# Optimization experiments

Hardware: AMD Instinct MI355X
Metric: run time of the kernel (lower is better)

## Reference

```python
import jax, jax.numpy as jnp
import numpy as np

C_IN, C_OUT, K, STRIDE, PAD = 64, 64, 3, 1, 1


def setup_inputs() -> dict:
    key = jax.random.key(0)
    k0, k1, k2, k3, k4 = jax.random.split(key, 5)
    x = jax.random.normal(k0, (8, C_IN, 128, 128), jnp.float32)
    # offset conv: out_channels = 2*K*K (torch inits to 0; use small random for non-trivial offsets)
    w_off = jax.random.normal(k1, (2 * K * K, C_IN, K, K), jnp.float32) * 0.01
    b_off = jax.random.normal(k2, (2 * K * K,), jnp.float32) * 0.01
    w_conv = jax.random.normal(k3, (C_OUT, C_IN, K, K), jnp.float32) * float(1.0 / np.sqrt(C_IN * K * K))
    b_conv = jax.random.normal(k4, (C_OUT,), jnp.float32) * 0.01
    return {"x": x, "w_off": w_off, "b_off": b_off, "w_conv": w_conv, "b_conv": b_conv}


def _conv(x, w, b, stride):
    y = jax.lax.conv_general_dilated(
        x, w, (stride, stride), 'VALID', dimension_numbers=('NCHW', 'OIHW', 'NCHW'))
    return y + b[None, :, None, None]


def _deform_forward(x, w_off, b_off, w_conv, b_conv):
    n, c, H, W = x.shape
    ph = H + 2 * PAD  # padded (square) spatial size
    xp = jnp.pad(x, ((0, 0), (0, 0), (PAD, PAD), (PAD, PAD)))
    offset = _conv(xp, w_off, b_off, STRIDE)           # [n, 2*K*K, h, w]
    h, w = offset.shape[2], offset.shape[3]
    # channel layout in the torch code: first K*K channels = x (col) deltas, next K*K = y (row)
    off = offset.reshape(n, 2, K, K, h, w)             # [n, {x,y}, ki, kj, h, w]
    base = (PAD + STRIDE * jnp.arange(h)).astype(x.dtype)          # p_0 centers in padded coords
    rng = (jnp.arange(K) - (K - 1) // 2).astype(x.dtype)           # p_n kernel offsets
    cx = off[:, 0] + base[None, None, None, None, :] + rng[None, None, :, None, None]
    cy = off[:, 1] + base[None, None, None, :, None] + rng[None, :, None, None, None]
    # equivalent to grid*2/(ph-1)-1 clamped to [-1,1] with align_corners=True
    cx = jnp.clip(cx, 0.0, ph - 1)
    cy = jnp.clip(cy, 0.0, ph - 1)
    # reorder [n, ki, kj, h, w] -> [n, h, ki, w, kj] -> [n, h*K, w*K] (matches torch permutes)
    cx = cx.transpose(0, 3, 1, 4, 2).reshape(n, h * K, w * K)
    cy = cy.transpose(0, 3, 1, 4, 2).reshape(n, h * K, w * K)
    # bilinear sampling (grid_sample, align_corners=True)
    x0 = jnp.floor(cx); y0 = jnp.floor(cy)
    wx = cx - x0; wy = cy - y0
    x0i = x0.astype(jnp.int32); y0i = y0.astype(jnp.int32)
    x1i = jnp.minimum(x0i + 1, ph - 1); y1i = jnp.minimum(y0i + 1, ph - 1)
    xf = xp.reshape(n, c, ph * ph)
    gather = jax.vmap(lambda xb, ib: xb[:, ib])        # ([c, P], [Hk, Wk]) -> [c, Hk, Wk]
    g00 = gather(xf, y0i * ph + x0i)
    g01 = gather(xf, y0i * ph + x1i)
    g10 = gather(xf, y1i * ph + x0i)
    g11 = gather(xf, y1i * ph + x1i)
    wxb = wx[:, None]; wyb = wy[:, None]               # broadcast over channels
    samp = (g00 * (1 - wxb) * (1 - wyb) + g01 * wxb * (1 - wyb)
            + g10 * (1 - wxb) * wyb + g11 * wxb * wyb)  # [n, c, h*K, w*K]
    return _conv(samp, w_conv, b_conv, K)               # stride-K conv -> [n, C_OUT, h, w]


def reference(x, w_off, b_off, w_conv, b_conv):
    return _deform_forward(x, w_off, b_off, w_conv, b_conv)
```

## Files before the change

### kernel.cpp

```cpp
#include <hip/hip_runtime.h>
#include <hip/hip_bf16.h>


#define PH   130
#define CIN  64
#define COUT 64
#define WROWS 7
#define WCOLS 72
#define ROWB  (WCOLS * 128)
#define WINB  (WROWS * ROWB)

typedef __attribute__((ext_vector_type(8))) __bf16 bf16x8;
typedef __attribute__((ext_vector_type(4))) float  f32x4;

__device__ __forceinline__ short f2bf(float f) {
  return __builtin_bit_cast(short, __float2bfloat16(f));
}
__device__ __forceinline__ float blo(unsigned u) {
  return __builtin_bit_cast(float, u << 16);
}
__device__ __forceinline__ float bhi(unsigned u) {
  return __builtin_bit_cast(float, u & 0xffff0000u);
}
__device__ __forceinline__ unsigned packbf(float a, float b) {
  unsigned lo16 = (unsigned short)__builtin_bit_cast(unsigned short, __float2bfloat16(a));
  unsigned hi16 = (unsigned short)__builtin_bit_cast(unsigned short, __float2bfloat16(b));
  return lo16 | (hi16 << 16);
}

__global__ __launch_bounds__(256) void k_pad_prep(
    const float* __restrict__ x, const float* __restrict__ w_off,
    const float* __restrict__ w_conv, __hip_bfloat16* __restrict__ xpT,
    short* __restrict__ Bpack, short* __restrict__ wOffPack) {
  __shared__ __hip_bfloat16 tile[128 * 64];
  int bid = blockIdx.x;
  int tid = threadIdx.x;
  if (bid < 8 * PH) {
    int n = bid / PH;
    int y = bid % PH;
    bool interior = (y >= 1 && y <= 128);
    if (interior) {
      for (int i = tid; i < 2048; i += 256) {
        int c  = i >> 5;
        int w4 = (i & 31) << 2;
        float4 v = *(const float4*)(x + (((size_t)(n * 64 + c) * 128) + (y - 1)) * 128 + w4);
        int sw = (i & 7) << 3;
        tile[(w4 + 0) * 64 + (c ^ sw)] = __float2bfloat16(v.x);
        tile[(w4 + 1) * 64 + (c ^ sw)] = __float2bfloat16(v.y);
        tile[(w4 + 2) * 64 + (c ^ sw)] = __float2bfloat16(v.z);
        tile[(w4 + 3) * 64 + (c ^ sw)] = __float2bfloat16(v.w);
      }
    }
    __syncthreads();
    __hip_bfloat16* dst = xpT + (size_t)(n * PH + y) * PH * CIN;
    bool zrow = (y == 0 || y == PH - 1);
    for (int i = tid; i < 1040; i += 256) {
      int px = i >> 3;
      int c0 = (i & 7) << 3;
      uint4 v;
      if (zrow || px == 0 || px == PH - 1) {
        v = make_uint4(0u, 0u, 0u, 0u);
      } else {
        int pxi = px - 1;
        int c0s = c0 ^ (((pxi >> 2) & 7) << 3);
        v = *(const uint4*)&tile[pxi * 64 + c0s];
      }
      *(uint4*)(dst + (size_t)i * 8) = v;
    }
  } else {
    int t = (bid - 8 * PH) * 256 + tid;
    if (t < 18 * 4 * 64) {
      int lane = t & 63;
      int nt   = (t >> 6) & 3;
      int kk   = t >> 8;
      int co   = nt * 16 + (lane & 15);
      int kbase = kk * 32 + ((lane >> 4) << 3);
      short v[8];
#pragma unroll
      for (int i = 0; i < 8; ++i) {
        int k = kbase + i;
        v[i] = f2bf(w_conv[(size_t)(co * 64 + (k & 63)) * 9 + (k >> 6)]);
      }
      *(uint4*)(Bpack + (size_t)t * 8) = *(const uint4*)v;
    }
    int u = t - 18 * 4 * 64;
    if (u >= 0 && u < 18 * 2 * 64) {
      int lane = u & 63;
      int nt   = (u >> 6) & 1;
      int kk   = u >> 7;
      int co   = nt * 16 + (lane & 15);
      int kbase = kk * 32 + ((lane >> 4) << 3);
      short v[8];
#pragma unroll
      for (int i = 0; i < 8; ++i) {
        int k = kbase + i;
        v[i] = (co < 18) ? f2bf(w_off[(size_t)(co * 64 + (k & 63)) * 9 + (k >> 6)]) : (short)0;
      }
      *(uint4*)(wOffPack + (size_t)u * 8) = *(const uint4*)v;
    }
  }
}

__global__ __launch_bounds__(256, 2) void k_fused(
    const __hip_bfloat16* __restrict__ xpT, const short* __restrict__ Bpack,
    const short* __restrict__ wOffPack, const float* __restrict__ b_off,
    const float* __restrict__ b_conv, float* __restrict__ out) {
  __shared__ __attribute__((aligned(16))) char shraw[78912];
  char*  win     = shraw;
  float* offsLds = (float*)(shraw + WINB);
  int4*  metaLds = (int4*)(shraw + WINB + 5120);
  int*   tf      = (int*)(shraw + WINB + 5120 + 9216);
  float* olds    = (float*)shraw;

  int bid = blockIdx.x;
  int wh  = bid & 1;
  int h   = (bid >> 1) & 127;
  int n   = bid >> 8;
  int w0  = wh << 6;
  int tid = threadIdx.x, wv = tid >> 6, lane = tid & 63;
  int p = lane & 15, oct = lane >> 4;
  const char* xbB = (const char*)(xpT + (size_t)n * PH * PH * CIN);

  if (tid < 9) tf[tid] = 0;
  for (int i = tid; i < 4032; i += 256) {
    int rec = i >> 3, chunk = i & 7;
    int r = rec / WCOLS, c = rec - r * WCOLS;
    int wrow = h - 2 + r, wcol = w0 - 2 + c;
    if ((unsigned)wrow <= 129u && (unsigned)wcol <= 129u) {
      uint4 v = *(const uint4*)(xbB + (size_t)(wrow * 130 + wcol) * 128 + chunk * 16);
      *(uint4*)(win + rec * 128 + ((chunk * 16) ^ ((c & 7) << 4))) = v;
    }
  }
  __syncthreads();

  {
    f32x4 ao0 = {0.f, 0.f, 0.f, 0.f}, ao1 = ao0;
    const bf16x8* Wo = (const bf16x8*)wOffPack;
    int colbase = 2 + wv * 16 + p;
#pragma unroll
    for (int kk = 0; kk < 18; ++kk) {
      int tap = kk >> 1;
      int ky = tap / 3, kx = tap - (tap / 3) * 3;
      int sub = kk & 1;
      int col = colbase + kx;
      int addr = (2 + ky) * ROWB + col * 128 + ((oct * 16 + sub * 64) ^ ((col & 7) << 4));
      bf16x8 a  = *(const bf16x8*)(win + addr);
      bf16x8 b0 = Wo[(kk * 2 + 0) * 64 + lane];
      bf16x8 b1 = Wo[(kk * 2 + 1) * 64 + lane];
      ao0 = __builtin_amdgcn_mfma_f32_16x16x32_bf16(a, b0, ao0, 0, 0, 0);
      ao1 = __builtin_amdgcn_mfma_f32_16x16x32_bf16(a, b1, ao1, 0, 0, 0);
    }
    int co = lane & 15;
    float bo0 = b_off[co];
#pragma unroll
    for (int r = 0; r < 4; ++r)
      offsLds[(wv * 16 + oct * 4 + r) * 20 + co] = ao0[r] + bo0;
    if (co < 2) {
      float bo1 = b_off[16 + co];
#pragma unroll
      for (int r = 0; r < 4; ++r)
        offsLds[(wv * 16 + oct * 4 + r) * 20 + 16 + co] = ao1[r] + bo1;
    }
  }
  __syncthreads();

  for (int t = tid; t < 576; t += 256) {
    int pix = t / 9, tap = t - pix * 9;
    int ky = tap / 3, kx = tap - (tap / 3) * 3;
    float cx = offsLds[pix * 20 + tap]     + (float)(w0 + pix + kx);
    float cy = offsLds[pix * 20 + 9 + tap] + (float)(h + ky);
    cx = fminf(fmaxf(cx, 0.f), 129.f);
    cy = fminf(fmaxf(cy, 0.f), 129.f);
    float x0f = floorf(cx), y0f = floorf(cy);
    int x0i = (int)x0f, y0i = (int)y0f;
    float wx = cx - x0f, wy = cy - y0f;
    int x1i = min(x0i + 1, 129), y1i = min(y0i + 1, 129);
    int x0r = x0i - w0 + 2, y0r = y0i - h + 2;
    int x1r = x1i - w0 + 2, y1r = y1i - h + 2;
    bool inw = (x0r >= 0) && (y0r >= 0) && (x1r <= WCOLS - 1) && (y1r <= WROWS - 1);
    if (!inw) atomicOr(&tf[tap], 1);
    int dxr = x1i - x0i, dyr = y1i - y0i;
    int rec00 = (y0r * WCOLS + x0r) & 511;
    metaLds[t] = make_int4((y0i * 130 + x0i) << 7, __builtin_bit_cast(int, wx),
                           __builtin_bit_cast(int, wy),
                           rec00 | (dxr << 9) | (dyr << 10));
  }
  __syncthreads();

  f32x4 acc0 = {0.f, 0.f, 0.f, 0.f}, acc1 = acc0, acc2 = acc0, acc3 = acc0;
  const bf16x8* Bp = (const bf16x8*)Bpack;
  int mbase = (wv * 16 + p) * 9;
  int innerQ = oct * 16;
  for (int tap = 0; tap < 9; ++tap) {
    int tfv = tf[tap];
    int4 mt = metaLds[mbase + tap];
    float wx = __builtin_bit_cast(float, mt.y);
    float wy = __builtin_bit_cast(float, mt.z);
    float w11 = wx * wy;
    float w01 = wx - w11;
    float w10 = wy - w11;
    float w00 = 1.f - wx - w10;
    int wrd = mt.w;
    int dxr = (wrd >> 9) & 1, dyr = (wrd >> 10) & 1;
    int a00 = 0, a01 = 0, a10 = 0, a11 = 0;
    const char* pb = nullptr;
    int dx = 0, dy = 0;
    if (tfv == 0) {
      int r00 = wrd & 511;
      int r01 = r00 + dxr, r10 = r00 + WCOLS * dyr, r11 = r10 + dxr;
      a00 = r00 * 128 + (innerQ ^ ((r00 & 7) << 4));
      a01 = r01 * 128 + (innerQ ^ ((r01 & 7) << 4));
      a10 = r10 * 128 + (innerQ ^ ((r10 & 7) << 4));
      a11 = r11 * 128 + (innerQ ^ ((r11 & 7) << 4));
    } else {
      pb = xbB + mt.x + (oct << 4);
      dx = dxr << 7;
      dy = dyr * 16640;
    }
#pragma unroll
    for (int half = 0; half < 2; ++half) {
      uint4 q00, q01, q10, q11;
      if (tfv == 0) {
        int hx = half << 6;
        q00 = *(const uint4*)(win + (a00 ^ hx));
        q01 = *(const uint4*)(win + (a01 ^ hx));
        q10 = *(const uint4*)(win + (a10 ^ hx));
        q11 = *(const uint4*)(win + (a11 ^ hx));
      } else {
        const char* pc = pb + (half << 6);
        q00 = *(const uint4*)(pc);
        q01 = *(const uint4*)(pc + dx);
        q10 = *(const uint4*)(pc + dy);
        q11 = *(const uint4*)(pc + dx + dy);
      }
      unsigned av[4];
#pragma unroll
      for (int j = 0; j < 4; ++j) {
        unsigned u00 = ((const unsigned*)&q00)[j];
        unsigned u01 = ((const unsigned*)&q01)[j];
        unsigned u10 = ((const unsigned*)&q10)[j];
        unsigned u11 = ((const unsigned*)&q11)[j];
        float sl = blo(u00) * w00 + blo(u01) * w01 + blo(u10) * w10 + blo(u11) * w11;
        float sh = bhi(u00) * w00 + bhi(u01) * w01 + bhi(u10) * w10 + bhi(u11) * w11;
        av[j] = packbf(sl, sh);
      }
      bf16x8 a = __builtin_bit_cast(bf16x8, *(uint4*)av);
      int kk = tap * 2 + half;
      bf16x8 b0 = Bp[(kk * 4 + 0) * 64 + lane];
      bf16x8 b1 = Bp[(kk * 4 + 1) * 64 + lane];
      bf16x8 b2 = Bp[(kk * 4 + 2) * 64 + lane];
      bf16x8 b3 = Bp[(kk * 4 + 3) * 64 + lane];
      acc0 = __builtin_amdgcn_mfma_f32_16x16x32_bf16(a, b0, acc0, 0, 0, 0);
      acc1 = __builtin_amdgcn_mfma_f32_16x16x32_bf16(a, b1, acc1, 0, 0, 0);
      acc2 = __builtin_amdgcn_mfma_f32_16x16x32_bf16(a, b2, acc2, 0, 0, 0);
      acc3 = __builtin_amdgcn_mfma_f32_16x16x32_bf16(a, b3, acc3, 0, 0, 0);
    }
  }
  __syncthreads();

  int prow0 = wv * 16 + (oct << 2);
#pragma unroll
  for (int r = 0; r < 4; ++r) {
    olds[(prow0 + r) * 68 + p     ] = acc0[r];
    olds[(prow0 + r) * 68 + p + 16] = acc1[r];
    olds[(prow0 + r) * 68 + p + 32] = acc2[r];
    olds[(prow0 + r) * 68 + p + 48] = acc3[r];
  }
  __syncthreads();
  float* ob = out + (size_t)n * COUT * 16384 + (size_t)h * 128 + w0;
  for (int i = tid; i < 4096; i += 256) {
    int co = i >> 6, px = i & 63;
    ob[(size_t)co * 16384 + px] = olds[px * 68 + co] + b_conv[co];
  }
}

extern "C" void kernel_launch(void* const* d_in, const int* in_sizes, int n_in,
                              void* d_out, int out_size, void* d_ws, size_t ws_size,
                              hipStream_t stream) {
  const float* x      = (const float*)d_in[0];
  const float* w_off  = (const float*)d_in[1];
  const float* b_off  = (const float*)d_in[2];
  const float* w_conv = (const float*)d_in[3];
  const float* b_conv = (const float*)d_in[4];
  float* out = (float*)d_out;

  char* ws = (char*)d_ws;
  __hip_bfloat16* xpT = (__hip_bfloat16*)ws;
  short* Bpack    = (short*)(ws + 17305600);
  short* wOffPack = (short*)(ws + 17305600 + 73728);

  k_pad_prep<<<dim3(8 * PH + 27), dim3(256), 0, stream>>>(x, w_off, w_conv,
                                                          xpT, Bpack, wOffPack);
  k_fused<<<dim3(2048), dim3(256), 0, stream>>>(xpT, Bpack, wOffPack, b_off, b_conv, out);
}
```

Before: 166.1 us.

## Shrink LDS window and metadata to fit three blocks per CU

Reduces the staged input window from 7 to 5 rows and stores offsets as bf16 and per-tap metadata as packed int2 with fp16 weights. Fallback flags become a single bitmask, which cuts LDS from about 79KB to 53KB so the launch bound can rise to 3 blocks per CU for more latency hiding. In exchange, offsets that leave the ±1-row window fall back to global gathers more often. The bf16 offset and fp16 weight storage also adds small precision loss.

```diff
diff --git a/kernel.cpp b/kernel.cpp
--- a/kernel.cpp
+++ b/kernel.cpp
@@ -5,7 +5,7 @@
 #define PH   130
 #define CIN  64
 #define COUT 64
-#define WROWS 7
+#define WROWS 5
 #define WCOLS 72
 #define ROWB  (WCOLS * 128)
 #define WINB  (WROWS * ROWB)
@@ -26,6 +26,12 @@
   unsigned lo16 = (unsigned short)__builtin_bit_cast(unsigned short, __float2bfloat16(a));
   unsigned hi16 = (unsigned short)__builtin_bit_cast(unsigned short, __float2bfloat16(b));
   return lo16 | (hi16 << 16);
+}
+__device__ __forceinline__ unsigned short f2h(float f) {
+  return __builtin_bit_cast(unsigned short, (_Float16)f);
+}
+__device__ __forceinline__ float h2f(unsigned short h) {
+  return (float)__builtin_bit_cast(_Float16, h);
 }
 
 __global__ __launch_bounds__(256) void k_pad_prep(
@@ -101,15 +107,15 @@
   }
 }
 
-__global__ __launch_bounds__(256, 2) void k_fused(
+__global__ __launch_bounds__(256, 3) void k_fused(
     const __hip_bfloat16* __restrict__ xpT, const short* __restrict__ Bpack,
     const short* __restrict__ wOffPack, const float* __restrict__ b_off,
     const float* __restrict__ b_conv, float* __restrict__ out) {
-  __shared__ __attribute__((aligned(16))) char shraw[78912];
+  __shared__ __attribute__((aligned(16))) char shraw[53264];
   char*  win     = shraw;
-  float* offsLds = (float*)(shraw + WINB);
-  int4*  metaLds = (int4*)(shraw + WINB + 5120);
-  int*   tf      = (int*)(shraw + WINB + 5120 + 9216);
+  __hip_bfloat16* offsB = (__hip_bfloat16*)(shraw + WINB);
+  int2*  metaLds = (int2*)(shraw + WINB + 2560);
+  int*   tf      = (int*)(shraw + WINB + 2560 + 4608);
   float* olds    = (float*)shraw;
 
   int bid = blockIdx.x;
@@ -121,11 +127,11 @@
   int p = lane & 15, oct = lane >> 4;
   const char* xbB = (const char*)(xpT + (size_t)n * PH * PH * CIN);
 
-  if (tid < 9) tf[tid] = 0;
-  for (int i = tid; i < 4032; i += 256) {
+  if (tid == 0) tf[0] = 0;
+  for (int i = tid; i < 2880; i += 256) {
     int rec = i >> 3, chunk = i & 7;
     int r = rec / WCOLS, c = rec - r * WCOLS;
-    int wrow = h - 2 + r, wcol = w0 - 2 + c;
+    int wrow = h - 1 + r, wcol = w0 - 2 + c;
     if ((unsigned)wrow <= 129u && (unsigned)wcol <= 129u) {
       uint4 v = *(const uint4*)(xbB + (size_t)(wrow * 130 + wcol) * 128 + chunk * 16);
       *(uint4*)(win + rec * 128 + ((chunk * 16) ^ ((c & 7) << 4))) = v;
@@ -143,7 +149,7 @@
       int ky = tap / 3, kx = tap - (tap / 3) * 3;
       int sub = kk & 1;
       int col = colbase + kx;
-      int addr = (2 + ky) * ROWB + col * 128 + ((oct * 16 + sub * 64) ^ ((col & 7) << 4));
+      int addr = (1 + ky) * ROWB + col * 128 + ((oct * 16 + sub * 64) ^ ((col & 7) << 4));
       bf16x8 a  = *(const bf16x8*)(win + addr);
       bf16x8 b0 = Wo[(kk * 2 + 0) * 64 + lane];
       bf16x8 b1 = Wo[(kk * 2 + 1) * 64 + lane];
@@ -154,12 +160,12 @@
     float bo0 = b_off[co];
 #pragma unroll
     for (int r = 0; r < 4; ++r)
-      offsLds[(wv * 16 + oct * 4 + r) * 20 + co] = ao0[r] + bo0;
+      offsB[(wv * 16 + oct * 4 + r) * 20 + co] = __float2bfloat16(ao0[r] + bo0);
     if (co < 2) {
       float bo1 = b_off[16 + co];
 #pragma unroll
       for (int r = 0; r < 4; ++r)
-        offsLds[(wv * 16 + oct * 4 + r) * 20 + 16 + co] = ao1[r] + bo1;
+        offsB[(wv * 16 + oct * 4 + r) * 20 + 16 + co] = __float2bfloat16(ao1[r] + bo1);
     }
   }
   __syncthreads();
@@ -167,23 +173,23 @@
   for (int t = tid; t < 576; t += 256) {
     int pix = t / 9, tap = t - pix * 9;
     int ky = tap / 3, kx = tap - (tap / 3) * 3;
-    float cx = offsLds[pix * 20 + tap]     + (float)(w0 + pix + kx);
-    float cy = offsLds[pix * 20 + 9 + tap] + (float)(h + ky);
+    float cx = __bfloat162float(offsB[pix * 20 + tap])     + (float)(w0 + pix + kx);
+    float cy = __bfloat162float(offsB[pix * 20 + 9 + tap]) + (float)(h + ky);
     cx = fminf(fmaxf(cx, 0.f), 129.f);
     cy = fminf(fmaxf(cy, 0.f), 129.f);
     float x0f = floorf(cx), y0f = floorf(cy);
     int x0i = (int)x0f, y0i = (int)y0f;
     float wx = cx - x0f, wy = cy - y0f;
     int x1i = min(x0i + 1, 129), y1i = min(y0i + 1, 129);
-    int x0r = x0i - w0 + 2, y0r = y0i - h + 2;
-    int x1r = x1i - w0 + 2, y1r = y1i - h + 2;
+    int x0r = x0i - w0 + 2, y0r = y0i - h + 1;
+    int x1r = x1i - w0 + 2, y1r = y1i - h + 1;
     bool inw = (x0r >= 0) && (y0r >= 0) && (x1r <= WCOLS - 1) && (y1r <= WROWS - 1);
-    if (!inw) atomicOr(&tf[tap], 1);
+    if (!inw) atomicOr(&tf[0], 1 << tap);
     int dxr = x1i - x0i, dyr = y1i - y0i;
     int rec00 = (y0r * WCOLS + x0r) & 511;
-    metaLds[t] = make_int4((y0i * 130 + x0i) << 7, __builtin_bit_cast(int, wx),
-                           __builtin_bit_cast(int, wy),
-                           rec00 | (dxr << 9) | (dyr << 10));
+    int w0rd = rec00 | (dxr << 9) | (dyr << 10) | (x0i << 12) | (y0i << 20);
+    int w1rd = (unsigned)f2h(wx) | ((unsigned)f2h(wy) << 16);
+    metaLds[t] = make_int2(w0rd, w1rd);
   }
   __syncthreads();
 
@@ -191,16 +197,18 @@
   const bf16x8* Bp = (const bf16x8*)Bpack;
   int mbase = (wv * 16 + p) * 9;
   int innerQ = oct * 16;
+  int fb = tf[0];
+#pragma unroll 1
   for (int tap = 0; tap < 9; ++tap) {
-    int tfv = tf[tap];
-    int4 mt = metaLds[mbase + tap];
-    float wx = __builtin_bit_cast(float, mt.y);
-    float wy = __builtin_bit_cast(float, mt.z);
+    int tfv = (fb >> tap) & 1;
+    int2 mt = metaLds[mbase + tap];
+    float wx = h2f((unsigned short)(mt.y & 0xffff));
+    float wy = h2f((unsigned short)((unsigned)mt.y >> 16));
     float w11 = wx * wy;
     float w01 = wx - w11;
     float w10 = wy - w11;
     float w00 = 1.f - wx - w10;
-    int wrd = mt.w;
+    int wrd = mt.x;
     int dxr = (wrd >> 9) & 1, dyr = (wrd >> 10) & 1;
     int a00 = 0, a01 = 0, a10 = 0, a11 = 0;
     const char* pb = nullptr;
@@ -213,7 +221,8 @@
       a10 = r10 * 128 + (innerQ ^ ((r10 & 7) << 4));
       a11 = r11 * 128 + (innerQ ^ ((r11 & 7) << 4));
     } else {
-      pb = xbB + mt.x + (oct << 4);
+      int x0i = (wrd >> 12) & 255, y0i = (wrd >> 20) & 255;
+      pb = xbB + ((y0i * 130 + x0i) << 7) + (oct << 4);
       dx = dxr << 7;
       dy = dyr * 16640;
     }
```

New measurement: 147.2 us. 11.4% less time.
